# Optimization experiments

Measured on AMD Instinct MI355X. Metric: run time of the kernel, lower is better.

## Reference

```python
import jax, jax.numpy as jnp
import numpy as np

BATCH, SEQ, DIM = 4, 4096, 2048
NUM_EXPERTS, TOP_K, RANK = 8, 2, 16
SCALING = 1.0


def setup_inputs() -> dict:
    key = jax.random.key(0)
    k0, k1, k2, k3 = jax.random.split(key, 4)
    s = 0.02
    x = jax.random.normal(k0, (BATCH, SEQ, DIM), dtype=jnp.float32)
    gate_W = jax.random.normal(k1, (NUM_EXPERTS, DIM), dtype=jnp.float32) * s  # [E, D] torch Linear layout
    gate_b = jnp.zeros((NUM_EXPERTS,), dtype=jnp.float32)
    A = jax.random.normal(k2, (NUM_EXPERTS, RANK, DIM), dtype=jnp.float32) * s   # lora_A weights [E, R, D]
    Bm = jax.random.normal(k3, (NUM_EXPERTS, DIM, RANK), dtype=jnp.float32) * s  # lora_B weights [E, D, R]
    return {"x": x, "gate_W": gate_W, "gate_b": gate_b, "A": A, "Bm": Bm}


def reference(x, gate_W, gate_b, A, Bm):
    # Gate: logits [B, S, E], softmax probs
    logits = jnp.einsum('bsd,ed->bse', x, gate_W) + gate_b
    gate_probs = jax.nn.softmax(logits, axis=-1)
    # Top-k selection. NOTE: the original torch code computes topk weights but
    # NEVER uses them -- expert outputs are summed unweighted over the top-k set.
    _, idx = jax.lax.top_k(gate_probs, TOP_K)  # idx: [B, S, K]
    # mask[b,s,e] = expert e is in token (b,s)'s top-k
    mask = jnp.any(idx[..., :, None] == jnp.arange(NUM_EXPERTS), axis=-2)  # [B, S, E] bool
    # Dense grouped LoRA: h [B, S, E, R] (small, rank=16), masked before combine
    h = jnp.einsum('bsd,erd->bser', x, A)
    h = jax.nn.gelu(h, approximate=False) * mask[..., None].astype(x.dtype)
    out = jnp.einsum('bser,edr->bsd', h, Bm) * SCALING  # [B, S, D]
    return out, gate_probs
```

## Files before the change

kernel.cpp:

```cpp
#include <hip/hip_runtime.h>
#include <math.h>

#define NTOK 16384
#define DIM  2048
#define NEXP 8
#define RANK 16

typedef unsigned short ushort_t;
typedef unsigned int   uint_t;
typedef __attribute__((ext_vector_type(8))) short bf16x8;
typedef __attribute__((ext_vector_type(4))) float f32x4;

__device__ __forceinline__ ushort_t f2bf(float f) {
  union { float f; uint_t u; } v; v.f = f;
  uint_t r = (v.u + 0x7FFFu + ((v.u >> 16) & 1u)) >> 16;
  return (ushort_t)r;
}
__device__ __forceinline__ float bf2f(ushort_t s) {
  union { uint_t u; float f; } v; v.u = ((uint_t)s) << 16;
  return v.f;
}

__device__ __forceinline__ void gl_lds16(const ushort_t* g, ushort_t* l) {
  __builtin_amdgcn_global_load_lds(
      (const __attribute__((address_space(1))) unsigned int*)g,
      (__attribute__((address_space(3))) unsigned int*)l, 16, 0, 0);
}

__global__ __launch_bounds__(256) void k0_prep(
    const float* __restrict__ gW, const float* __restrict__ A,
    const float* __restrict__ Bm,
    ushort_t* __restrict__ Wc, ushort_t* __restrict__ Bm2) {
  int b = blockIdx.x, t = threadIdx.x;
  if (b < 1280) {
    int idx = b * 256 + t;
    int r = idx >> 11, d = idx & 2047;
    float v;
    if (r < 8)        v = gW[r * 2048 + d];
    else if (r < 16)  v = 0.f;
    else if (r < 144) v = A[(size_t)(r - 16) * 2048 + d];
    else if (r < 152) { float g = gW[(r - 144) * 2048 + d]; v = g - bf2f(f2bf(g)); }
    else              v = 0.f;
    int ch = d >> 6, c = d & 63;
    int cs = ((((c >> 3) ^ (r & 7)) << 3) | (c & 7));
    Wc[((size_t)ch * 160 + r) * 64 + cs] = f2bf(v);
  } else {
    int idx = (b - 1280) * 256 + t;
    int dd = idx >> 7, c = idx & 127, e = c >> 4, rr = c & 15;
    Bm2[idx] = f2bf(Bm[((size_t)e * 2048 + dd) * 16 + rr]);
  }
}

#define BKP 72

__global__ __launch_bounds__(256) void k1_fused(
    const float* __restrict__ x, const float* __restrict__ gate_b,
    const ushort_t* __restrict__ Wc, const ushort_t* __restrict__ Bm2,
    float* __restrict__ out, float* __restrict__ probs) {
  __shared__ __align__(16) ushort_t ws_w[2][160 * 64];
  __shared__ __align__(16) ushort_t xs_hi[2][32][BKP];
  __shared__ __align__(16) ushort_t xs_lo[2][32][BKP];
  __shared__ float Cs[32][152];
  __shared__ int sel0s[32], sel1s[32];
  ushort_t* hm_s = &ws_w[0][0];

  const int t = threadIdx.x;
  const int lane = t & 63, wave = t >> 6;
  const int l15 = lane & 15, q = lane >> 4;
  const int mt = wave & 1;
  const int ng = wave >> 1;
  const int ntiles = ng ? 5 : 4;
  const int tok0 = blockIdx.x * 32;

  f32x4 acc[5];
  #pragma unroll
  for (int i = 0; i < 5; ++i) acc[i] = (f32x4)0.f;

  const float4* xg = (const float4*)(x + (size_t)tok0 * DIM);
  const int xrow0 = t >> 4, xc4 = t & 15;

  float4 xv[2];

  auto load_x = [&](int ch) {
    xv[0] = xg[xrow0 * (DIM / 4) + ch * 16 + xc4];
    xv[1] = xg[(16 + xrow0) * (DIM / 4) + ch * 16 + xc4];
  };
  auto stage_w = [&](int ch, int buf) {
    const ushort_t* src = Wc + (size_t)ch * (160 * 64);
    #pragma unroll
    for (int i = 0; i < 5; ++i)
      gl_lds16(src + (size_t)(i * 256 + t) * 8,
               &ws_w[buf][(i * 256 + wave * 64) * 8]);
  };
  auto write_x = [&](int buf) {
    #pragma unroll
    for (int i = 0; i < 2; ++i) {
      int row = xrow0 + i * 16;
      float vv[4] = {xv[i].x, xv[i].y, xv[i].z, xv[i].w};
      ushort_t h4[4], l4[4];
      #pragma unroll
      for (int j = 0; j < 4; ++j) {
        h4[j] = f2bf(vv[j]);
        l4[j] = f2bf(vv[j] - bf2f(h4[j]));
      }
      *(uint2*)&xs_hi[buf][row][xc4 * 4] = *(const uint2*)h4;
      *(uint2*)&xs_lo[buf][row][xc4 * 4] = *(const uint2*)l4;
    }
  };

  load_x(0);
  stage_w(0, 0);
  write_x(0);
  __syncthreads();

  for (int ch = 0; ch < 32; ++ch) {
    const int cur = ch & 1, nxt = cur ^ 1;
    if (ch < 31) { load_x(ch + 1); stage_w(ch + 1, nxt); }

    const ushort_t* wb = ws_w[cur];
    auto wfrag = [&](int r, int kkg) -> bf16x8 {
      int pos = (r << 3) + ((kkg + q) ^ (r & 7));
      return *(const bf16x8*)&wb[pos << 3];
    };

    #pragma unroll
    for (int kk = 0; kk < 64; kk += 32) {
      const int kkg = kk >> 3;
      bf16x8 ah = *(const bf16x8*)&xs_hi[cur][mt * 16 + l15][kk + q * 8];
      if (ng == 0) {
        bf16x8 al  = *(const bf16x8*)&xs_lo[cur][mt * 16 + l15][kk + q * 8];
        bf16x8 bgl = wfrag(144 + l15, kkg);
        bf16x8 b0  = wfrag(l15, kkg);
        acc[0] = __builtin_amdgcn_mfma_f32_16x16x32_bf16(ah, b0, acc[0], 0, 0, 0);
        acc[0] = __builtin_amdgcn_mfma_f32_16x16x32_bf16(al, b0, acc[0], 0, 0, 0);
        acc[0] = __builtin_amdgcn_mfma_f32_16x16x32_bf16(ah, bgl, acc[0], 0, 0, 0);
        #pragma unroll
        for (int nt = 1; nt < 4; ++nt) {
          bf16x8 b = wfrag(nt * 16 + l15, kkg);
          acc[nt] = __builtin_amdgcn_mfma_f32_16x16x32_bf16(ah, b, acc[nt], 0, 0, 0);
        }
      } else {
        #pragma unroll
        for (int nt = 0; nt < 5; ++nt) {
          bf16x8 b = wfrag(64 + nt * 16 + l15, kkg);
          acc[nt] = __builtin_amdgcn_mfma_f32_16x16x32_bf16(ah, b, acc[nt], 0, 0, 0);
        }
      }
    }

    if (ch < 31) write_x(nxt);
    __syncthreads();
  }

  const int colbase = ng ? 64 : 0;
  #pragma unroll
  for (int i = 0; i < 5; ++i) {
    if (i < ntiles) {
      #pragma unroll
      for (int r = 0; r < 4; ++r)
        Cs[mt * 16 + q * 4 + r][colbase + i * 16 + l15] = acc[i][r];
    }
  }
  __syncthreads();

  if (t < 32) {
    int m = t;
    float lg[NEXP];
    #pragma unroll
    for (int e = 0; e < NEXP; ++e) lg[e] = Cs[m][e] + gate_b[e];
    float mx = lg[0];
    #pragma unroll
    for (int e = 1; e < NEXP; ++e) mx = fmaxf(mx, lg[e]);
    float ex[NEXP], s = 0.f;
    #pragma unroll
    for (int e = 0; e < NEXP; ++e) { ex[e] = __expf(lg[e] - mx); s += ex[e]; }
    float inv = 1.f / s;
    float4 p0 = make_float4(ex[0] * inv, ex[1] * inv, ex[2] * inv, ex[3] * inv);
    float4 p1 = make_float4(ex[4] * inv, ex[5] * inv, ex[6] * inv, ex[7] * inv);
    float* pp = probs + (size_t)(tok0 + m) * NEXP;
    *(float4*)pp = p0; *(float4*)(pp + 4) = p1;
    int i0 = 0;
    #pragma unroll
    for (int e = 1; e < NEXP; ++e) if (lg[e] > lg[i0]) i0 = e;
    int i1 = (i0 == 0) ? 1 : 0;
    #pragma unroll
    for (int e = 0; e < NEXP; ++e) if (e != i0 && lg[e] > lg[i1]) i1 = e;
    sel0s[m] = i0; sel1s[m] = i1;
  }
  __syncthreads();

  {
    int m = t >> 3, e = t & 7;
    int on = (e == sel0s[m]) | (e == sel1s[m]);
    ushort_t ov[16];
    #pragma unroll
    for (int r = 0; r < RANK; ++r) {
      float v = Cs[m][16 + e * 16 + r];
      float g = on ? (0.5f * v * (1.f + erff(v * 0.70710678118654752f))) : 0.f;
      ov[r] = f2bf(g);
    }
    int g0 = (2 * e) ^ (m & 7), g1 = (2 * e + 1) ^ (m & 7);
    *(uint4*)&hm_s[m * 128 + g0 * 8] = *(const uint4*)&ov[0];
    *(uint4*)&hm_s[m * 128 + g1 * 8] = *(const uint4*)&ov[8];
  }
  __syncthreads();

  {
    bf16x8 af[2][4];
    #pragma unroll
    for (int m2 = 0; m2 < 2; ++m2) {
      int tok = m2 * 16 + l15;
      #pragma unroll
      for (int kk = 0; kk < 4; ++kk)
        af[m2][kk] = *(const bf16x8*)&hm_s[tok * 128 + (((kk * 4 + q) ^ (tok & 7)) << 3)];
    }

    const int ncol0 = wave * 512;
    const ushort_t* bp = Bm2 + (size_t)(ncol0 + l15) * 128 + q * 8;

    auto loadB = [&](bf16x8* dst, int i) {
      #pragma unroll
      for (int k = 0; k < 4; ++k)
        dst[k] = *(const bf16x8*)(bp + (size_t)i * 2048 + k * 32);
    };
    auto comp = [&](const bf16x8* bb, int i) {
      #pragma unroll
      for (int m2 = 0; m2 < 2; ++m2) {
        f32x4 c = (f32x4)0.f;
        #pragma unroll
        for (int k = 0; k < 4; ++k)
          c = __builtin_amdgcn_mfma_f32_16x16x32_bf16(bb[k], af[m2][k], c, 0, 0, 0);
        *(f32x4*)&out[(size_t)(tok0 + m2 * 16 + l15) * DIM + ncol0 + i * 16 + q * 4] = c;
      }
    };

    bf16x8 bA[4], bB[4];
    loadB(bA, 0);
    #pragma unroll
    for (int ii = 0; ii < 16; ++ii) {
      loadB(bB, 2 * ii + 1);
      comp(bA, 2 * ii);
      if (ii < 15) loadB(bA, 2 * ii + 2);
      comp(bB, 2 * ii + 1);
    }
  }
}

extern "C" void kernel_launch(void* const* d_in, const int* in_sizes, int n_in,
                              void* d_out, int out_size, void* d_ws, size_t ws_size,
                              hipStream_t stream) {
  const float* x      = (const float*)d_in[0];
  const float* gate_W = (const float*)d_in[1];
  const float* gate_b = (const float*)d_in[2];
  const float* A      = (const float*)d_in[3];
  const float* Bm     = (const float*)d_in[4];

  float* out   = (float*)d_out;
  float* probs = out + (size_t)NTOK * DIM;

  ushort_t* Wc  = (ushort_t*)d_ws;
  ushort_t* Bm2 = Wc + 32 * 160 * 64;

  k0_prep<<<dim3(2304), dim3(256), 0, stream>>>(gate_W, A, Bm, Wc, Bm2);
  k1_fused<<<dim3(NTOK / 32), dim3(256), 0, stream>>>(x, gate_b, Wc, Bm2, out, probs);
}
```

Measured before the change: 275.9 us.

## Double workgroup size to 512 threads and redistribute tiles across eight waves

Raises the fused kernel from 4 to 8 waves per 32-token block. The gate/LoRA-A MFMA tiles are split into 2–3 per wave, x loading and W staging are spread over more threads, and each wave covers half as many output columns in the LoRA-B stage. The goal is more latency hiding and parallelism per block while the LDS footprint stays the same. In exchange, each wave does fewer MFMAs between barriers, and the 512-thread blocks may limit occupancy through register pressure.

After: 277.7 us. Within noise of the previous version (+0.7%).

```diff
diff --git a/kernel.cpp b/kernel.cpp
--- a/kernel.cpp
+++ b/kernel.cpp
@@ -53,7 +53,7 @@
 
 #define BKP 72
 
-__global__ __launch_bounds__(256) void k1_fused(
+__global__ __launch_bounds__(512) void k1_fused(
     const float* __restrict__ x, const float* __restrict__ gate_b,
     const ushort_t* __restrict__ Wc, const ushort_t* __restrict__ Bm2,
     float* __restrict__ out, float* __restrict__ probs) {
@@ -69,43 +69,37 @@
   const int l15 = lane & 15, q = lane >> 4;
   const int mt = wave & 1;
   const int ng = wave >> 1;
-  const int ntiles = ng ? 5 : 4;
+  const int tile0 = (ng == 3) ? 6 : ng * 2;
+  const int ntiles = (ng == 3) ? 3 : 2;
   const int tok0 = blockIdx.x * 32;
 
-  f32x4 acc[5];
+  f32x4 acc[3];
   #pragma unroll
-  for (int i = 0; i < 5; ++i) acc[i] = (f32x4)0.f;
+  for (int i = 0; i < 3; ++i) acc[i] = (f32x4)0.f;
 
   const float4* xg = (const float4*)(x + (size_t)tok0 * DIM);
-  const int xrow0 = t >> 4, xc4 = t & 15;
-
-  float4 xv[2];
+  const int xrow = t >> 4, xc4 = t & 15;
+
+  float4 xv;
 
   auto load_x = [&](int ch) {
-    xv[0] = xg[xrow0 * (DIM / 4) + ch * 16 + xc4];
-    xv[1] = xg[(16 + xrow0) * (DIM / 4) + ch * 16 + xc4];
+    xv = xg[xrow * (DIM / 4) + ch * 16 + xc4];
   };
   auto stage_w = [&](int ch, int buf) {
     const ushort_t* src = Wc + (size_t)ch * (160 * 64);
-    #pragma unroll
-    for (int i = 0; i < 5; ++i)
-      gl_lds16(src + (size_t)(i * 256 + t) * 8,
-               &ws_w[buf][(i * 256 + wave * 64) * 8]);
+    for (int i = wave; i < 20; i += 8)
+      gl_lds16(src + (size_t)(i * 64 + lane) * 8, &ws_w[buf][i * 512]);
   };
   auto write_x = [&](int buf) {
-    #pragma unroll
-    for (int i = 0; i < 2; ++i) {
-      int row = xrow0 + i * 16;
-      float vv[4] = {xv[i].x, xv[i].y, xv[i].z, xv[i].w};
-      ushort_t h4[4], l4[4];
-      #pragma unroll
-      for (int j = 0; j < 4; ++j) {
-        h4[j] = f2bf(vv[j]);
-        l4[j] = f2bf(vv[j] - bf2f(h4[j]));
-      }
-      *(uint2*)&xs_hi[buf][row][xc4 * 4] = *(const uint2*)h4;
-      *(uint2*)&xs_lo[buf][row][xc4 * 4] = *(const uint2*)l4;
-    }
+    float vv[4] = {xv.x, xv.y, xv.z, xv.w};
+    ushort_t h4[4], l4[4];
+    #pragma unroll
+    for (int j = 0; j < 4; ++j) {
+      h4[j] = f2bf(vv[j]);
+      l4[j] = f2bf(vv[j] - bf2f(h4[j]));
+    }
+    *(uint2*)&xs_hi[buf][xrow][xc4 * 4] = *(const uint2*)h4;
+    *(uint2*)&xs_lo[buf][xrow][xc4 * 4] = *(const uint2*)l4;
   };
 
   load_x(0);
@@ -134,16 +128,15 @@
         acc[0] = __builtin_amdgcn_mfma_f32_16x16x32_bf16(ah, b0, acc[0], 0, 0, 0);
         acc[0] = __builtin_amdgcn_mfma_f32_16x16x32_bf16(al, b0, acc[0], 0, 0, 0);
         acc[0] = __builtin_amdgcn_mfma_f32_16x16x32_bf16(ah, bgl, acc[0], 0, 0, 0);
-        #pragma unroll
-        for (int nt = 1; nt < 4; ++nt) {
-          bf16x8 b = wfrag(nt * 16 + l15, kkg);
-          acc[nt] = __builtin_amdgcn_mfma_f32_16x16x32_bf16(ah, b, acc[nt], 0, 0, 0);
-        }
+        bf16x8 b1 = wfrag(16 + l15, kkg);
+        acc[1] = __builtin_amdgcn_mfma_f32_16x16x32_bf16(ah, b1, acc[1], 0, 0, 0);
       } else {
         #pragma unroll
-        for (int nt = 0; nt < 5; ++nt) {
-          bf16x8 b = wfrag(64 + nt * 16 + l15, kkg);
-          acc[nt] = __builtin_amdgcn_mfma_f32_16x16x32_bf16(ah, b, acc[nt], 0, 0, 0);
+        for (int i = 0; i < 3; ++i) {
+          if (i < ntiles) {
+            bf16x8 b = wfrag((tile0 + i) * 16 + l15, kkg);
+            acc[i] = __builtin_amdgcn_mfma_f32_16x16x32_bf16(ah, b, acc[i], 0, 0, 0);
+          }
         }
       }
     }
@@ -152,13 +145,12 @@
     __syncthreads();
   }
 
-  const int colbase = ng ? 64 : 0;
   #pragma unroll
-  for (int i = 0; i < 5; ++i) {
+  for (int i = 0; i < 3; ++i) {
     if (i < ntiles) {
       #pragma unroll
       for (int r = 0; r < 4; ++r)
-        Cs[mt * 16 + q * 4 + r][colbase + i * 16 + l15] = acc[i][r];
+        Cs[mt * 16 + q * 4 + r][(tile0 + i) * 16 + l15] = acc[i][r];
     }
   }
   __syncthreads();
@@ -189,7 +181,7 @@
   }
   __syncthreads();
 
-  {
+  if (t < 256) {
     int m = t >> 3, e = t & 7;
     int on = (e == sel0s[m]) | (e == sel1s[m]);
     ushort_t ov[16];
@@ -215,7 +207,7 @@
         af[m2][kk] = *(const bf16x8*)&hm_s[tok * 128 + (((kk * 4 + q) ^ (tok & 7)) << 3)];
     }
 
-    const int ncol0 = wave * 512;
+    const int ncol0 = wave * 256;
     const ushort_t* bp = Bm2 + (size_t)(ncol0 + l15) * 128 + q * 8;
 
     auto loadB = [&](bf16x8* dst, int i) {
@@ -237,10 +229,10 @@
     bf16x8 bA[4], bB[4];
     loadB(bA, 0);
     #pragma unroll
-    for (int ii = 0; ii < 16; ++ii) {
+    for (int ii = 0; ii < 8; ++ii) {
       loadB(bB, 2 * ii + 1);
       comp(bA, 2 * ii);
-      if (ii < 15) loadB(bA, 2 * ii + 2);
+      if (ii < 7) loadB(bA, 2 * ii + 2);
       comp(bB, 2 * ii + 1);
     }
   }
@@ -262,5 +254,5 @@
   ushort_t* Bm2 = Wc + 32 * 160 * 64;
 
   k0_prep<<<dim3(2304), dim3(256), 0, stream>>>(gate_W, A, Bm, Wc, Bm2);
-  k1_fused<<<dim3(NTOK / 32), dim3(256), 0, stream>>>(x, gate_b, Wc, Bm2, out, probs);
-}
+  k1_fused<<<dim3(NTOK / 32), dim3(512), 0, stream>>>(x, gate_b, Wc, Bm2, out, probs);
+}
```
